# Kernel optimization log

Hardware: AMD Instinct MI355X
Metric: run time of the kernel (lower is better)

## Reference

```python
import jax, jax.numpy as jnp
import numpy as np

B, S, D = 4, 4096, 768  # batch, seq_len, n_units
NEG = -1000000000.0      # masked_fill value from the torch source


def setup_inputs() -> dict:
    key = jax.random.key(0)
    ks = jax.random.split(key, 12)
    scale = 1.0 / np.sqrt(D)
    inp = {
        "query": jax.random.normal(ks[0], (B, S, D), jnp.float32),
        "key_": jax.random.normal(ks[1], (B, S, D), jnp.float32),
        "value": jax.random.normal(ks[2], (B, S, D), jnp.float32),
        # nn.Linear weights are [out, in]; forward computes x @ W.T + b
        "Wq": jax.random.normal(ks[3], (D, D), jnp.float32) * scale,
        "bq": jnp.zeros((D,), jnp.float32),
        "Wk": jax.random.normal(ks[4], (D, D), jnp.float32) * scale,
        "bk": jnp.zeros((D,), jnp.float32),
        "Wv": jax.random.normal(ks[5], (D, D), jnp.float32) * scale,
        "bv": jnp.zeros((D,), jnp.float32),
        "Wo": jax.random.normal(ks[6], (D, D), jnp.float32) * scale,
        "bo": jnp.zeros((D,), jnp.float32),
        # broadcastable causal mask [1, S, S]; 0 -> masked
        "mask": jnp.tril(jnp.ones((S, S), jnp.int32))[None, :, :],
    }
    return inp


def reference(query, key_, value, Wq, bq, Wk, bk, Wv, bv, Wo, bo, mask):
    # QKV projections (torch Linear: x @ W.T + b)
    q = jnp.einsum("bsd,ed->bse", query, Wq) + bq
    k = jnp.einsum("bsd,ed->bse", key_, Wk) + bk
    v = jnp.einsum("bsd,ed->bse", value, Wv) + bv
    # scores: NOTE source scales by n_units**0.5 (full model dim, no head split)
    weights = jnp.einsum("bqd,bkd->bqk", q, k) / jnp.sqrt(jnp.float32(D))
    weights = jnp.where(mask == 0, jnp.float32(NEG), weights)
    weights = jax.nn.softmax(weights, axis=-1)
    # dropout is identity in eval/deterministic reference
    attended = jnp.einsum("bqk,bkd->bqd", weights, v)
    return jnp.einsum("bsd,ed->bse", attended, Wo) + bo
```

## Files before the change

### kernel.cpp

```cpp
#include <hip/hip_runtime.h>
#include <hip/hip_bf16.h>
#include <stdint.h>

#define DI __device__ __forceinline__

typedef __bf16 bf16x4 __attribute__((ext_vector_type(4)));
typedef __bf16 bf16x8 __attribute__((ext_vector_type(8)));
typedef float  f32x4  __attribute__((ext_vector_type(4)));

static constexpr int  BATCH = 4;
static constexpr int  SEQ   = 4096;
static constexpr int  DIM   = 768;
static constexpr long TOK   = (long)BATCH * SEQ;
static constexpr int  QT    = SEQ / 128;
static constexpr int  NTRI  = QT * (QT + 1) / 2;
static constexpr float SCALE = 0.0360843918243516150f;

__global__ void cvt4_kernel(const float* __restrict__ a, const float* __restrict__ b,
                            const float* __restrict__ c, const float* __restrict__ d,
                            __bf16* __restrict__ oa, __bf16* __restrict__ ob,
                            __bf16* __restrict__ oc, __bf16* __restrict__ od, long n4){
  const float* in  = blockIdx.y == 0 ? a : blockIdx.y == 1 ? b : blockIdx.y == 2 ? c : d;
  __bf16*      out = blockIdx.y == 0 ? oa : blockIdx.y == 1 ? ob : blockIdx.y == 2 ? oc : od;
  long i = (long)blockIdx.x * blockDim.x + threadIdx.x;
  const long stride = (long)gridDim.x * blockDim.x;
  for(; i < n4; i += stride){
    float4 v = ((const float4*)in)[i];
    bf16x4 o = { (__bf16)v.x, (__bf16)v.y, (__bf16)v.z, (__bf16)v.w };
    ((bf16x4*)out)[i] = o;
  }
}

DI int swz_off(int r, int c){ return (r << 7) + ((c ^ (r & 7)) << 4); }

template<int R>
DI void stage(const __bf16* __restrict__ src, long ld, char* lds, int tid){
  const int w = tid >> 6, l = tid & 63;
  const int rsub = l >> 3;
  const int kc   = (l & 7) ^ rsub;
  const __bf16* g = src + (long)(w * 8 + rsub) * ld + kc * 8;
  char* d = lds + (w << 10);
  #pragma unroll
  for(int i = 0; i < R / 64; ++i){
    __builtin_amdgcn_global_load_lds(
        (const __attribute__((address_space(1))) void*)(g + (long)(i * 64) * ld),
        (__attribute__((address_space(3))) void*)(d + i * 8192), 16, 0, 0);
  }
}

template<int R>
DI void stage_cvt(const float* __restrict__ src, long ld, char* lds, int tid){
  const int w = tid >> 6, l = tid & 63;
  const int rsub = l >> 3;
  const int kc   = (l & 7) ^ rsub;
  const float* g = src + (long)(w * 8 + rsub) * ld + kc * 8;
  char* d = lds + (w << 10) + (l << 4);
  #pragma unroll
  for(int i = 0; i < R / 64; ++i){
    const float4* s = (const float4*)(g + (long)(i * 64) * ld);
    float4 v0 = s[0], v1 = s[1];
    bf16x8 o = { (__bf16)v0.x, (__bf16)v0.y, (__bf16)v0.z, (__bf16)v0.w,
                 (__bf16)v1.x, (__bf16)v1.y, (__bf16)v1.z, (__bf16)v1.w };
    *(bf16x8*)(d + i * 8192) = o;
  }
}

template<int R>
DI void stage_add(const __bf16* __restrict__ a0, const __bf16* __restrict__ a1,
                  long ld, char* lds, int tid){
  const int w = tid >> 6, l = tid & 63;
  const int rsub = l >> 3;
  const int kc   = (l & 7) ^ rsub;
  const long off = (long)(w * 8 + rsub) * ld + kc * 8;
  char* d = lds + (w << 10) + (l << 4);
  #pragma unroll
  for(int i = 0; i < R / 64; ++i){
    bf16x8 v0 = *(const bf16x8*)(a0 + off + (long)(i * 64) * ld);
    bf16x8 v1 = *(const bf16x8*)(a1 + off + (long)(i * 64) * ld);
    bf16x8 o;
    #pragma unroll
    for(int e = 0; e < 8; ++e) o[e] = (__bf16)((float)v0[e] + (float)v1[e]);
    *(bf16x8*)(d + i * 8192) = o;
  }
}

DI bf16x8 frag_ld(const char* lds, int row, int c){
  return *(const bf16x8*)(lds + swz_off(row, c));
}

DI void mma_tile(const char* As, const char* Bs, int lane, int wr, int wc, f32x4 acc[4][4]){
  #pragma unroll
  for(int kk = 0; kk < 2; ++kk){
    const int c = kk * 4 + (lane >> 4);
    bf16x8 a[4], b[4];
    #pragma unroll
    for(int i = 0; i < 4; ++i) a[i] = frag_ld(As, wr + i * 16 + (lane & 15), c);
    #pragma unroll
    for(int j = 0; j < 4; ++j) b[j] = frag_ld(Bs, wc + j * 16 + (lane & 15), c);
    #pragma unroll
    for(int i = 0; i < 4; ++i)
      #pragma unroll
      for(int j = 0; j < 4; ++j)
        acc[i][j] = __builtin_amdgcn_mfma_f32_16x16x32_bf16(a[i], b[j], acc[i][j], 0, 0, 0);
  }
}

template<class FA, class FB>
DI void kloop2(FA fa, long lda, FB fb, long ldb, int nt, int tid,
               char* As, char* Bs, f32x4 acc[4][4]){
  const int lane = tid & 63, w = tid >> 6;
  const int wr = (w >> 2) * 64, wc = (w & 3) * 64;
  for(int t = 0; t < nt; ++t){
    stage<128>(fa(t), lda, As, tid);
    stage<256>(fb(t), ldb, Bs, tid);
    __syncthreads();
    mma_tile(As, Bs, lane, wr, wc, acc);
    __syncthreads();
  }
}

__global__ __launch_bounds__(512)
void proj_qkv(const float* __restrict__ query, const float* __restrict__ key_,
              const float* __restrict__ value, const __bf16* __restrict__ Wqb,
              const __bf16* __restrict__ Wkb, const __bf16* __restrict__ Wvb,
              const float* __restrict__ bq, const float* __restrict__ bk,
              const float* __restrict__ bv, __bf16* __restrict__ qb,
              __bf16* __restrict__ kb, __bf16* __restrict__ vbT){
  __shared__ __attribute__((aligned(128))) char As[16384];
  __shared__ __attribute__((aligned(128))) char Bs[32768];
  const int z = blockIdx.y, bid = blockIdx.x, tid = threadIdx.x;
  const int lane = tid & 63, w = tid >> 6;
  const int wr = (w >> 2) * 64, wc = (w & 3) * 64;
  f32x4 acc[4][4] = {};
  const int cl = lane & 15, rq = (lane >> 4) * 4;

  if(z < 2){
    const float*  X = z ? key_ : query;
    const __bf16* W = z ? Wkb : Wqb;
    const float*  bias = z ? bk : bq;
    __bf16*       C = z ? kb : qb;
    const long m0 = (long)(bid / 3) * 128, n0 = (bid % 3) * 256;
    const float*  Ar = X + m0 * DIM;
    const __bf16* Br = W + n0 * DIM;
    for(int t = 0; t < DIM / 64; ++t){
      stage_cvt<128>(Ar + t * 64, DIM, As, tid);
      stage<256>(Br + t * 64, DIM, Bs, tid);
      __syncthreads();
      mma_tile(As, Bs, lane, wr, wc, acc);
      __syncthreads();
    }
    #pragma unroll
    for(int i = 0; i < 4; ++i)
      #pragma unroll
      for(int j = 0; j < 4; ++j){
        const long gc = n0 + wc + j * 16 + cl;
        #pragma unroll
        for(int e = 0; e < 4; ++e){
          const long gr = m0 + wr + i * 16 + rq + e;
          C[gr * DIM + gc] = (__bf16)(acc[i][j][e] + bias[gc]);
        }
      }
  } else {
    const long m0 = (long)(bid / 64) * 128, n0 = (long)(bid % 64) * 256;
    const __bf16* Ar = Wvb + m0 * DIM;
    const float*  Br = value + n0 * DIM;
    for(int t = 0; t < DIM / 64; ++t){
      stage<128>(Ar + t * 64, DIM, As, tid);
      stage_cvt<256>(Br + t * 64, DIM, Bs, tid);
      __syncthreads();
      mma_tile(As, Bs, lane, wr, wc, acc);
      __syncthreads();
    }
    #pragma unroll
    for(int i = 0; i < 4; ++i)
      #pragma unroll
      for(int j = 0; j < 4; ++j){
        const long gc = n0 + wc + j * 16 + cl;
        #pragma unroll
        for(int e = 0; e < 4; ++e){
          const long gr = m0 + wr + i * 16 + rq + e;
          vbT[gr * TOK + gc] = (__bf16)(acc[i][j][e] + bv[gr]);
        }
      }
  }
}

__global__ __launch_bounds__(512)
void qk_kernel(const __bf16* __restrict__ qb, const __bf16* __restrict__ kb,
               __bf16* __restrict__ Pc, float* __restrict__ rlsum){
  const int b = blockIdx.y, t2 = blockIdx.x, tid = threadIdx.x;
  int Qi = (int)((sqrtf(4.0f * t2 + 1.0f) - 1.0f) * 0.5f);
  while((Qi + 1) * (Qi + 2) <= t2) Qi++;
  while(Qi * (Qi + 1) > t2) Qi--;
  const int ki = t2 - Qi * (Qi + 1);
  const __bf16* Aq = qb + ((long)b * SEQ + Qi * 256) * DIM;
  const __bf16* Bk = kb + ((long)b * SEQ + ki * 128) * DIM;
  __shared__ __attribute__((aligned(128))) char As[32768];
  __shared__ __attribute__((aligned(128))) char Bs[16384];
  const int lane = tid & 63, w = tid >> 6;
  const int wr = (w >> 1) * 64, wc = (w & 1) * 64;
  f32x4 acc[4][4] = {};
  for(int t = 0; t < DIM / 64; ++t){
    stage<256>(Aq + t * 64, DIM, As, tid);
    stage<128>(Bk + t * 64, DIM, Bs, tid);
    __syncthreads();
    mma_tile(As, Bs, lane, wr, wc, acc);
    __syncthreads();
  }
  const int cl = lane & 15, rq = (lane >> 4) * 4;
  #pragma unroll
  for(int i = 0; i < 4; ++i){
    const int rbase = wr + i * 16;
    const int qi = 2 * Qi + (rbase >> 7);
    if(ki > qi) continue;
    const bool diag = (ki == qi);
    __bf16* tile = Pc + ((long)b * NTRI + (long)qi * (qi + 1) / 2 + ki) * 16384;
    float rsum[4] = {0.f, 0.f, 0.f, 0.f};
    #pragma unroll
    for(int j = 0; j < 4; ++j){
      const int c = wc + j * 16 + cl;
      #pragma unroll
      for(int e = 0; e < 4; ++e){
        const int rloc = (rbase + rq + e) & 127;
        float p = (diag && c > rloc) ? 0.0f
                  : __expf(fminf(acc[i][j][e] * SCALE, 30.0f));
        tile[rloc * 128 + c] = (__bf16)p;
        rsum[e] += p;
      }
    }
    #pragma unroll
    for(int e = 0; e < 4; ++e){
      float s = rsum[e];
      s += __shfl_xor(s, 1); s += __shfl_xor(s, 2);
      s += __shfl_xor(s, 4); s += __shfl_xor(s, 8);
      if(cl == 0){
        const long gr = (long)b * SEQ + Qi * 256 + rbase + rq + e;
        atomicAdd(&rlsum[gr], s);
      }
    }
  }
}

__global__ __launch_bounds__(512)
void pv_kernel(const __bf16* __restrict__ Pc, const float* __restrict__ rlsum,
               const __bf16* __restrict__ vbT, __bf16* __restrict__ att0,
               __bf16* __restrict__ att1){
  __shared__ __attribute__((aligned(128))) char As[16384];
  __shared__ __attribute__((aligned(128))) char Bs[32768];
  __shared__ float sRl[128];
  const int x = blockIdx.x, y = blockIdx.y, tid = threadIdx.x;
  const long n0 = (long)(x >> 2) * 256;
  const int b = x & 3;
  int qi, k0, k1, half;
  if(y == 62){ qi = 0; k0 = 0; k1 = 1; half = 0; }
  else{
    qi = 31 - (y >> 1); half = y & 1;
    const int c0 = (qi + 2) >> 1;
    if(half == 0){ k0 = 0; k1 = c0; } else { k0 = c0; k1 = qi + 1; }
  }
  if(tid < 128) sRl[tid] = 1.0f / rlsum[b * SEQ + qi * 128 + tid];
  const __bf16* Pq = Pc + ((long)b * NTRI + (long)qi * (qi + 1) / 2) * 16384;
  const __bf16* Bv = vbT + n0 * TOK + (long)b * SEQ;
  f32x4 acc[4][4] = {};
  auto fa = [&](int t){ return Pq + (long)(k0 + (t >> 1)) * 16384 + (t & 1) * 64; };
  auto fb = [&](int t){ return Bv + (long)k0 * 128 + t * 64; };
  kloop2(fa, 128, fb, TOK, 2 * (k1 - k0), tid, As, Bs, acc);

  __bf16* dst = half ? att1 : att0;
  const int lane = tid & 63, w = tid >> 6;
  const int wr = (w >> 2) * 64, wc = (w & 3) * 64;
  const int cl = lane & 15, rq = (lane >> 4) * 4;
  #pragma unroll
  for(int i = 0; i < 4; ++i)
    #pragma unroll
    for(int j = 0; j < 4; ++j){
      const long gc = n0 + wc + j * 16 + cl;
      #pragma unroll
      for(int e = 0; e < 4; ++e){
        const int rloc = wr + i * 16 + rq + e;
        float v = acc[i][j][e] * sRl[rloc];
        dst[((long)b * SEQ + qi * 128 + rloc) * DIM + gc] = (__bf16)v;
      }
    }
}

__global__ __launch_bounds__(512)
void oproj(const __bf16* __restrict__ att0, const __bf16* __restrict__ att1,
           const __bf16* __restrict__ Wob, const float* __restrict__ bo,
           float* __restrict__ out){
  __shared__ __attribute__((aligned(128))) char As[16384];
  __shared__ __attribute__((aligned(128))) char Bs[32768];
  const int bid = blockIdx.x, tid = threadIdx.x;
  const long n0 = (bid % 3) * 256, m0 = (long)(bid / 3) * 128;
  const __bf16* Br = Wob + n0 * DIM;
  f32x4 acc[4][4] = {};
  const int lane = tid & 63, w = tid >> 6;
  const int wr = (w >> 2) * 64, wc = (w & 3) * 64;
  for(int t = 0; t < DIM / 64; ++t){
    stage_add<128>(att0 + m0 * DIM + t * 64, att1 + m0 * DIM + t * 64, DIM, As, tid);
    stage<256>(Br + t * 64, DIM, Bs, tid);
    __syncthreads();
    mma_tile(As, Bs, lane, wr, wc, acc);
    __syncthreads();
  }
  const int cl = lane & 15, rq = (lane >> 4) * 4;
  #pragma unroll
  for(int i = 0; i < 4; ++i)
    #pragma unroll
    for(int j = 0; j < 4; ++j){
      const long gc = n0 + wc + j * 16 + cl;
      #pragma unroll
      for(int e = 0; e < 4; ++e){
        const long gr = m0 + wr + i * 16 + rq + e;
        out[gr * DIM + gc] = acc[i][j][e] + bo[gc];
      }
    }
}

extern "C" void kernel_launch(void* const* d_in, const int* in_sizes, int n_in,
                              void* d_out, int out_size, void* d_ws, size_t ws_size,
                              hipStream_t stream){
  const float* query = (const float*)d_in[0];
  const float* key_  = (const float*)d_in[1];
  const float* value = (const float*)d_in[2];
  const float* Wq = (const float*)d_in[3];
  const float* bq = (const float*)d_in[4];
  const float* Wk = (const float*)d_in[5];
  const float* bk = (const float*)d_in[6];
  const float* Wv = (const float*)d_in[7];
  const float* bv = (const float*)d_in[8];
  const float* Wo = (const float*)d_in[9];
  const float* bo = (const float*)d_in[10];

  char* p = (char*)d_ws;
  auto carve = [&](size_t bytes)->char*{
    char* r = p; p += (bytes + 255) & ~(size_t)255; return r;
  };
  const size_t tb = (size_t)TOK * DIM * 2;
  __bf16* qb   = (__bf16*)carve(tb);
  __bf16* kb   = (__bf16*)carve(tb);
  __bf16* vbT  = (__bf16*)carve(tb);
  __bf16* att0 = (__bf16*)carve(tb);
  __bf16* att1 = (__bf16*)carve(tb);
  __bf16* Wqb = (__bf16*)carve((size_t)DIM * DIM * 2);
  __bf16* Wkb = (__bf16*)carve((size_t)DIM * DIM * 2);
  __bf16* Wvb = (__bf16*)carve((size_t)DIM * DIM * 2);
  __bf16* Wob = (__bf16*)carve((size_t)DIM * DIM * 2);
  __bf16* Pc  = (__bf16*)carve((size_t)BATCH * NTRI * 16384 * 2);
  float*  rlr = (float*)carve((size_t)TOK * 4);
  if((size_t)(p - (char*)d_ws) > ws_size) return;

  const long nW4 = (long)DIM * DIM / 4;
  dim3 g4((unsigned)((nW4 + 255) / 256), 4);
  hipMemsetAsync(rlr, 0, (size_t)TOK * 4, stream);
  hipMemsetAsync(att1, 0, tb, stream);
  cvt4_kernel<<<g4, 256, 0, stream>>>(Wq, Wk, Wv, Wo, Wqb, Wkb, Wvb, Wob, nW4);

  proj_qkv<<<dim3(384, 3), 512, 0, stream>>>(query, key_, value, Wqb, Wkb, Wvb,
                                             bq, bk, bv, qb, kb, vbT);

  qk_kernel<<<dim3(272, BATCH), 512, 0, stream>>>(qb, kb, Pc, rlr);

  pv_kernel<<<dim3(12, 63), 512, 0, stream>>>(Pc, rlr, vbT, att0, att1);

  oproj<<<384, 512, 0, stream>>>(att0, att1, Wob, bo, (float*)d_out);
}
```

Measured before the change: 315.7 us.

## Prefetch next fp32 activation tile into registers during QKV projection MMA

Replaces the synchronous convert-then-stage loop in the QKV projection with a software-pipelined loop. The next k-step's fp32 activations are loaded into registers while the current tile is computed, with explicit waitcnt and barriers. The V projection also swaps its tile shape so the fp32 operand is the 128-row side, which halves the per-thread fp32 traffic in that path. This is meant to hide global load latency of the fp32 inputs, at the cost of extra registers and hand-written synchronization.

Result: slower. 333.8 us (+5.7%).

```diff
diff --git a/kernel.cpp b/kernel.cpp
--- a/kernel.cpp
+++ b/kernel.cpp
@@ -49,23 +49,6 @@
 }
 
 template<int R>
-DI void stage_cvt(const float* __restrict__ src, long ld, char* lds, int tid){
-  const int w = tid >> 6, l = tid & 63;
-  const int rsub = l >> 3;
-  const int kc   = (l & 7) ^ rsub;
-  const float* g = src + (long)(w * 8 + rsub) * ld + kc * 8;
-  char* d = lds + (w << 10) + (l << 4);
-  #pragma unroll
-  for(int i = 0; i < R / 64; ++i){
-    const float4* s = (const float4*)(g + (long)(i * 64) * ld);
-    float4 v0 = s[0], v1 = s[1];
-    bf16x8 o = { (__bf16)v0.x, (__bf16)v0.y, (__bf16)v0.z, (__bf16)v0.w,
-                 (__bf16)v1.x, (__bf16)v1.y, (__bf16)v1.z, (__bf16)v1.w };
-    *(bf16x8*)(d + i * 8192) = o;
-  }
-}
-
-template<int R>
 DI void stage_add(const __bf16* __restrict__ a0, const __bf16* __restrict__ a1,
                   long ld, char* lds, int tid){
   const int w = tid >> 6, l = tid & 63;
@@ -119,6 +102,45 @@
   }
 }
 
+template<int NT>
+DI void kloop_t14(const float* gf32, long ldf, char* dfw,
+                  const __bf16* gbf, long ldb, char* dbf,
+                  const char* LA, const char* LB,
+                  int lane, int wr, int wc, f32x4 acc[4][4]){
+  float4 p0, p1, p2, p3;
+  auto ldr = [&](int t){
+    const float* g0 = gf32 + t * 64;
+    const float* g1 = g0 + (long)64 * ldf;
+    p0 = ((const float4*)g0)[0]; p1 = ((const float4*)g0)[1];
+    p2 = ((const float4*)g1)[0]; p3 = ((const float4*)g1)[1];
+  };
+  ldr(0);
+  for(int t = 0; t < NT; ++t){
+    bf16x8 o0 = { (__bf16)p0.x, (__bf16)p0.y, (__bf16)p0.z, (__bf16)p0.w,
+                  (__bf16)p1.x, (__bf16)p1.y, (__bf16)p1.z, (__bf16)p1.w };
+    bf16x8 o1 = { (__bf16)p2.x, (__bf16)p2.y, (__bf16)p2.z, (__bf16)p2.w,
+                  (__bf16)p3.x, (__bf16)p3.y, (__bf16)p3.z, (__bf16)p3.w };
+    *(bf16x8*)dfw = o0;
+    *(bf16x8*)(dfw + 8192) = o1;
+    #pragma unroll
+    for(int i = 0; i < 4; ++i)
+      __builtin_amdgcn_global_load_lds(
+          (const __attribute__((address_space(1))) void*)(gbf + t * 64 + (long)(i * 64) * ldb),
+          (__attribute__((address_space(3))) void*)(dbf + i * 8192), 16, 0, 0);
+    asm volatile("" ::: "memory");
+    if(t + 1 < NT){
+      ldr(t + 1);
+      asm volatile("s_waitcnt vmcnt(4) lgkmcnt(0)" ::: "memory");
+    } else {
+      asm volatile("s_waitcnt vmcnt(0) lgkmcnt(0)" ::: "memory");
+    }
+    __builtin_amdgcn_s_barrier();
+    mma_tile(LA, LB, lane, wr, wc, acc);
+    asm volatile("" ::: "memory");
+    __builtin_amdgcn_s_barrier();
+  }
+}
+
 __global__ __launch_bounds__(512)
 void proj_qkv(const float* __restrict__ query, const float* __restrict__ key_,
               const float* __restrict__ value, const __bf16* __restrict__ Wqb,
@@ -126,13 +148,12 @@
               const float* __restrict__ bq, const float* __restrict__ bk,
               const float* __restrict__ bv, __bf16* __restrict__ qb,
               __bf16* __restrict__ kb, __bf16* __restrict__ vbT){
-  __shared__ __attribute__((aligned(128))) char As[16384];
-  __shared__ __attribute__((aligned(128))) char Bs[32768];
+  __shared__ __attribute__((aligned(128))) char L[49152];
   const int z = blockIdx.y, bid = blockIdx.x, tid = threadIdx.x;
-  const int lane = tid & 63, w = tid >> 6;
-  const int wr = (w >> 2) * 64, wc = (w & 3) * 64;
+  const int lane = tid & 63, w = tid >> 6, l = tid & 63;
+  const int rsub = l >> 3, kc = (l & 7) ^ rsub;
+  const int cl = lane & 15, rq = (lane >> 4) * 4;
   f32x4 acc[4][4] = {};
-  const int cl = lane & 15, rq = (lane >> 4) * 4;
 
   if(z < 2){
     const float*  X = z ? key_ : query;
@@ -140,15 +161,13 @@
     const float*  bias = z ? bk : bq;
     __bf16*       C = z ? kb : qb;
     const long m0 = (long)(bid / 3) * 128, n0 = (bid % 3) * 256;
-    const float*  Ar = X + m0 * DIM;
-    const __bf16* Br = W + n0 * DIM;
-    for(int t = 0; t < DIM / 64; ++t){
-      stage_cvt<128>(Ar + t * 64, DIM, As, tid);
-      stage<256>(Br + t * 64, DIM, Bs, tid);
-      __syncthreads();
-      mma_tile(As, Bs, lane, wr, wc, acc);
-      __syncthreads();
-    }
+    char* LA = L;
+    char* LB = L + 16384;
+    const float*  gf = X + (m0 + w * 8 + rsub) * DIM + kc * 8;
+    const __bf16* gb = W + (n0 + w * 8 + rsub) * DIM + kc * 8;
+    const int wr = (w >> 2) * 64, wc = (w & 3) * 64;
+    kloop_t14<DIM / 64>(gf, DIM, LA + (w << 10) + (l << 4),
+                        gb, DIM, LB + (w << 10), LA, LB, lane, wr, wc, acc);
     #pragma unroll
     for(int i = 0; i < 4; ++i)
       #pragma unroll
@@ -161,16 +180,14 @@
         }
       }
   } else {
-    const long m0 = (long)(bid / 64) * 128, n0 = (long)(bid % 64) * 256;
-    const __bf16* Ar = Wvb + m0 * DIM;
-    const float*  Br = value + n0 * DIM;
-    for(int t = 0; t < DIM / 64; ++t){
-      stage<128>(Ar + t * 64, DIM, As, tid);
-      stage_cvt<256>(Br + t * 64, DIM, Bs, tid);
-      __syncthreads();
-      mma_tile(As, Bs, lane, wr, wc, acc);
-      __syncthreads();
-    }
+    const long m0 = (long)(bid / 128) * 256, n0 = (long)(bid % 128) * 128;
+    char* LA = L;
+    char* LB = L + 32768;
+    const __bf16* ga = Wvb + (m0 + w * 8 + rsub) * DIM + kc * 8;
+    const float*  gf = value + (n0 + w * 8 + rsub) * DIM + kc * 8;
+    const int wr = (w >> 1) * 64, wc = (w & 1) * 64;
+    kloop_t14<DIM / 64>(gf, DIM, LB + (w << 10) + (l << 4),
+                        ga, DIM, LA + (w << 10), LA, LB, lane, wr, wc, acc);
     #pragma unroll
     for(int i = 0; i < 4; ++i)
       #pragma unroll
```
